# Kernel optimization log

Measured on AMD Instinct MI355X. Metric: run time of the kernel, lower is better.

The kernel has to match this reference:

```python
import jax, jax.numpy as jnp
import numpy as np

UNITS = 1024
NUM_HEADS = 8


def setup_inputs() -> dict:
    key = jax.random.key(0)
    k1, k2, k3 = jax.random.split(key, 3)
    B, S = 8, 1024
    memory = jax.random.normal(k1, (B, S, 2 * UNITS), dtype=jnp.float32)
    query = jax.random.normal(k2, (B, S, UNITS), dtype=jnp.float32)
    seq_mask = jax.random.randint(k3, (B, S), 0, 2, dtype=jnp.int32)
    b = jnp.zeros((1,), dtype=jnp.float32)  # learned scalar bias added to logits
    return {"memory": memory, "query": query, "seq_mask": seq_mask, "b": b}


def _split_heads(x, n):
    # [B, S, D] -> [B, n, S, D//n]
    B, S, D = x.shape
    return x.reshape(B, S, n, D // n).transpose(0, 2, 1, 3)


def reference(memory, query, seq_mask, b):
    H = NUM_HEADS
    depth = UNITS // H
    Q = _split_heads(query, H) * (depth ** -0.5)          # [B,H,S,d]
    k_mem, v_mem = jnp.split(memory, 2, axis=2)
    K = _split_heads(k_mem, H)                            # [B,H,S,d]
    V = _split_heads(v_mem, H)                            # [B,H,S,d]
    logits = jnp.einsum('bhqd,bhkd->bhqk', Q, K) + b[0]   # [B,H,S,S]
    mask = seq_mask.astype(jnp.float32)[:, None, None, :]  # [B,1,1,S]
    logits = logits + (-1e30) * (1.0 - mask)
    weights = jax.nn.softmax(logits, axis=-1)
    out = jnp.einsum('bhqk,bhkd->bhqd', weights, V)       # [B,H,S,d]
    B, _, S, _ = out.shape
    return out.transpose(0, 2, 1, 3).reshape(B, S, UNITS)
```

## Files before the change

### kernel.cpp

```cpp
#include <hip/hip_runtime.h>
#include <stdint.h>


typedef __attribute__((ext_vector_type(8))) short bf16x8;
typedef __attribute__((ext_vector_type(4))) float f32x4;
typedef __attribute__((ext_vector_type(16))) float f32x16;
typedef __attribute__((ext_vector_type(4))) unsigned int u32x4;

#define NB 8
#define SS 1024
#define NH 8
#define DH 128
#define BM 128
#define BN 64
#define KPAD 136
#define VPAD 72
#define NT (SS / BN)

__device__ __forceinline__ unsigned short f2bf(float f) {
    unsigned int u = __builtin_bit_cast(unsigned int, f);
    u += 0x7fffu + ((u >> 16) & 1u);
    return (unsigned short)(u >> 16);
}

__device__ __forceinline__ unsigned int cvt_pk_bf16(float lo, float hi) {
#if __has_builtin(__builtin_amdgcn_cvt_pk_bf16_f32)
    typedef __attribute__((ext_vector_type(2))) __bf16 bf16x2_t;
    bf16x2_t r = __builtin_amdgcn_cvt_pk_bf16_f32(lo, hi);
    return __builtin_bit_cast(unsigned int, r);
#else
    return (unsigned int)f2bf(lo) | ((unsigned int)f2bf(hi) << 16);
#endif
}

__device__ __forceinline__ void bar_lgkm() {
    asm volatile("s_waitcnt lgkmcnt(0)" ::: "memory");
    __builtin_amdgcn_s_barrier();
    asm volatile("" ::: "memory");
}

__device__ __forceinline__ void pswap(unsigned int &a, unsigned int &b) {
#if __has_builtin(__builtin_amdgcn_permlane32_swap)
    auto r = __builtin_amdgcn_permlane32_swap(a, b, false, false);
    a = (unsigned int)r[0];
    b = (unsigned int)r[1];
#else
    unsigned int sa = (unsigned int)__shfl_xor((int)a, 32, 64);
    unsigned int sb = (unsigned int)__shfl_xor((int)b, 32, 64);
    const bool hh = (threadIdx.x & 32) != 0;
    unsigned int na = hh ? sb : a;
    unsigned int nb = hh ? b : sa;
    a = na; b = nb;
#endif
}

__global__ __launch_bounds__(256, 2)
void attn_flash(const float* __restrict__ mem,
                const float* __restrict__ query,
                const int* __restrict__ seq_mask,
                float* __restrict__ out)
{
    __shared__ unsigned short K_lds[2][BN * KPAD];
    __shared__ unsigned short Vt_lds[2][DH * VPAD];

    const int tid  = threadIdx.x;
    const int wave = tid >> 6;
    const int lane = tid & 63;
    const int hi   = lane >> 5;
    const int l31  = lane & 31;

    const int bh = blockIdx.x;
    const int b  = bh >> 3;
    const int h  = bh & 7;
    const int q0w = blockIdx.y * BM + wave * 32;

    bf16x8 qf[8];
    {
        const float* qb = query + ((size_t)(b * SS + q0w + l31) << 10) + h * DH + hi * 8;
        #pragma unroll
        for (int dep = 0; dep < 8; ++dep) {
            f32x4 lo = *(const f32x4*)(qb + dep * 16);
            f32x4 ho = *(const f32x4*)(qb + dep * 16 + 4);
            u32x4 q;
            q[0] = cvt_pk_bf16(lo[0], lo[1]);
            q[1] = cvt_pk_bf16(lo[2], lo[3]);
            q[2] = cvt_pk_bf16(ho[0], ho[1]);
            q[3] = cvt_pk_bf16(ho[2], ho[3]);
            qf[dep] = __builtin_bit_cast(bf16x8, q);
        }
    }

    f32x16 acc[4];
    #pragma unroll
    for (int dt = 0; dt < 4; ++dt)
        #pragma unroll
        for (int i = 0; i < 16; ++i) acc[dt][i] = 0.f;
    float l_i = 0.f;

    const float cs = 0.12752789747141537f;

    const int krow = tid >> 4;
    const int kcc  = (tid & 15) * 8;
    const int vq   = tid & 31;
    const int vg8  = tid >> 5;

    const float* kbase = mem + ((size_t)(b * SS) << 11) + h * DH;
    const float* vbase = kbase + 1024;
    const int* mbase = seq_mask + b * SS;

    f32x4 pka[4], pkb[4];
    f32x4 pva0[2], pva1[2], pvb0[2], pvb1[2];
    int pmv, pmv_next;

    #pragma unroll
    for (int it = 0; it < 4; ++it) {
        const float* src = kbase + ((size_t)(it * 16 + krow) << 11) + kcc;
        pka[it] = *(const f32x4*)src;
        pkb[it] = *(const f32x4*)(src + 4);
    }
    #pragma unroll
    for (int task = 0; task < 2; ++task) {
        int d0 = vg8 * 8 + task * 64;
        const float* pa = vbase + ((size_t)(2 * vq) << 11) + d0;
        pva0[task] = *(const f32x4*)pa;
        pva1[task] = *(const f32x4*)(pa + 4);
        pvb0[task] = *(const f32x4*)(pa + 2048);
        pvb1[task] = *(const f32x4*)(pa + 2048 + 4);
    }
    pmv = mbase[lane];

    #pragma unroll
    for (int it = 0; it < 4; ++it) {
        u32x4 t;
        t[0] = cvt_pk_bf16(pka[it][0], pka[it][1]);
        t[1] = cvt_pk_bf16(pka[it][2], pka[it][3]);
        t[2] = cvt_pk_bf16(pkb[it][0], pkb[it][1]);
        t[3] = cvt_pk_bf16(pkb[it][2], pkb[it][3]);
        *(u32x4*)&K_lds[0][(it * 16 + krow) * KPAD + kcc] = t;
    }
    #pragma unroll
    for (int task = 0; task < 2; ++task) {
        int d0 = vg8 * 8 + task * 64;
        #pragma unroll
        for (int j = 0; j < 8; ++j) {
            float av = (j < 4) ? pva0[task][j] : pva1[task][j - 4];
            float bv = (j < 4) ? pvb0[task][j] : pvb1[task][j - 4];
            *(unsigned int*)&Vt_lds[0][(d0 + j) * VPAD + 2 * vq] =
                cvt_pk_bf16(av, bv);
        }
    }

    #pragma unroll
    for (int it = 0; it < 4; ++it) {
        const float* src = kbase + ((size_t)(BN + it * 16 + krow) << 11) + kcc;
        pka[it] = *(const f32x4*)src;
        pkb[it] = *(const f32x4*)(src + 4);
    }
    #pragma unroll
    for (int task = 0; task < 2; ++task) {
        int d0 = vg8 * 8 + task * 64;
        const float* pa = vbase + ((size_t)(BN + 2 * vq) << 11) + d0;
        pva0[task] = *(const f32x4*)pa;
        pva1[task] = *(const f32x4*)(pa + 4);
        pvb0[task] = *(const f32x4*)(pa + 2048);
        pvb1[task] = *(const f32x4*)(pa + 2048 + 4);
    }
    pmv_next = mbase[BN + lane];

    bar_lgkm();

    for (int kt = 0; kt < NT; ++kt) {
        const int cur = kt & 1;
        const unsigned short* Kc = &K_lds[cur][0];
        const unsigned short* Vc = &Vt_lds[cur][0];

        const unsigned long long bmask = __ballot(pmv != 0);
        const unsigned int wsh0 = (unsigned int)(bmask >> (4 * hi));
        const unsigned int wsh1 = (unsigned int)(bmask >> (32 + 4 * hi));

        #pragma unroll
        for (int jt = 0; jt < 2; ++jt) {
            const unsigned int mword = jt ? wsh1 : wsh0;

            f32x16 s;
            #pragma unroll
            for (int i = 0; i < 16; ++i) s[i] = 0.f;
            __builtin_amdgcn_s_setprio(1);
            #pragma unroll
            for (int dep = 0; dep < 8; ++dep) {
                bf16x8 kf = *(const bf16x8*)&Kc[(jt * 32 + l31) * KPAD + dep * 16 + hi * 8];
                s = __builtin_amdgcn_mfma_f32_32x32x16_bf16(kf, qf[dep], s, 0, 0, 0);
            }
            __builtin_amdgcn_s_setprio(0);

            float p[16];
            #pragma unroll
            for (int r = 0; r < 16; ++r) {
                const int sr = (r & 3) + 8 * (r >> 2);
                float e = __builtin_amdgcn_exp2f(s[r] * cs);
                float m = (float)((mword >> sr) & 1u);
                p[r] = e * m;
            }
            {
                float t0 = (p[0] + p[1]) + (p[2] + p[3]);
                float t1 = (p[4] + p[5]) + (p[6] + p[7]);
                float t2 = (p[8] + p[9]) + (p[10] + p[11]);
                float t3 = (p[12] + p[13]) + (p[14] + p[15]);
                l_i += (t0 + t1) + (t2 + t3);
            }

            unsigned int w[8];
            #pragma unroll
            for (int i = 0; i < 8; ++i) w[i] = cvt_pk_bf16(p[2 * i], p[2 * i + 1]);
            pswap(w[0], w[2]); pswap(w[1], w[3]);
            pswap(w[4], w[6]); pswap(w[5], w[7]);
            bf16x8 af0 = __builtin_bit_cast(bf16x8, (u32x4){w[0], w[1], w[2], w[3]});
            bf16x8 af1 = __builtin_bit_cast(bf16x8, (u32x4){w[4], w[5], w[6], w[7]});

            __builtin_amdgcn_s_setprio(1);
            #pragma unroll
            for (int ksl = 0; ksl < 2; ++ksl) {
                bf16x8 ap = ksl ? af1 : af0;
                #pragma unroll
                for (int dt = 0; dt < 4; ++dt) {
                    bf16x8 bv = *(const bf16x8*)&Vc[(dt * 32 + l31) * VPAD +
                                                    jt * 32 + ksl * 16 + hi * 8];
                    acc[dt] = __builtin_amdgcn_mfma_f32_32x32x16_bf16(ap, bv, acc[dt], 0, 0, 0);
                }
            }
            __builtin_amdgcn_s_setprio(0);
        }

        if (kt < NT - 1) {
            unsigned short* Kn = &K_lds[cur ^ 1][0];
            unsigned short* Vn = &Vt_lds[cur ^ 1][0];
            #pragma unroll
            for (int it = 0; it < 4; ++it) {
                u32x4 t;
                t[0] = cvt_pk_bf16(pka[it][0], pka[it][1]);
                t[1] = cvt_pk_bf16(pka[it][2], pka[it][3]);
                t[2] = cvt_pk_bf16(pkb[it][0], pkb[it][1]);
                t[3] = cvt_pk_bf16(pkb[it][2], pkb[it][3]);
                *(u32x4*)&Kn[(it * 16 + krow) * KPAD + kcc] = t;
            }
            #pragma unroll
            for (int task = 0; task < 2; ++task) {
                int d0 = vg8 * 8 + task * 64;
                #pragma unroll
                for (int j = 0; j < 8; ++j) {
                    float av = (j < 4) ? pva0[task][j] : pva1[task][j - 4];
                    float bv = (j < 4) ? pvb0[task][j] : pvb1[task][j - 4];
                    *(unsigned int*)&Vn[(d0 + j) * VPAD + 2 * vq] =
                        cvt_pk_bf16(av, bv);
                }
            }

            const int kk2 = (kt < NT - 2) ? (kt + 2) * BN : (kt + 1) * BN;
            #pragma unroll
            for (int it = 0; it < 4; ++it) {
                const float* src = kbase + ((size_t)(kk2 + it * 16 + krow) << 11) + kcc;
                pka[it] = *(const f32x4*)src;
                pkb[it] = *(const f32x4*)(src + 4);
            }
            #pragma unroll
            for (int task = 0; task < 2; ++task) {
                int d0 = vg8 * 8 + task * 64;
                const float* pa = vbase + ((size_t)(kk2 + 2 * vq) << 11) + d0;
                pva0[task] = *(const f32x4*)pa;
                pva1[task] = *(const f32x4*)(pa + 4);
                pvb0[task] = *(const f32x4*)(pa + 2048);
                pvb1[task] = *(const f32x4*)(pa + 2048 + 4);
            }
            pmv = pmv_next;
            pmv_next = mbase[kk2 + lane];

            bar_lgkm();
        }
    }

    float lt = l_i + __shfl_xor(l_i, 32, 64);
    float invl = 1.f / lt;
    #pragma unroll
    for (int r = 0; r < 16; ++r) {
        const int qrow = (r & 3) + 8 * (r >> 2) + 4 * hi;
        float iv = __shfl(invl, qrow, 64);
        float* ob = out + ((size_t)(b * SS + q0w + qrow) << 10) + h * DH + l31;
        #pragma unroll
        for (int dt = 0; dt < 4; ++dt)
            ob[dt * 32] = acc[dt][r] * iv;
    }
}

extern "C" void kernel_launch(void* const* d_in, const int* in_sizes, int n_in,
                              void* d_out, int out_size, void* d_ws, size_t ws_size,
                              hipStream_t stream)
{
    (void)in_sizes; (void)n_in; (void)d_ws; (void)ws_size; (void)out_size;
    const float* mem    = (const float*)d_in[0];
    const float* query  = (const float*)d_in[1];
    const int* seq_mask = (const int*)d_in[2];
    dim3 grid(NB * NH, SS / BM);
    attn_flash<<<grid, 256, 0, stream>>>(mem, query, seq_mask, (float*)d_out);
}
```

Baseline: 176.2 us.

## Move key masking into V tiles and compute softmax denominator via MFMA

Masked keys are now handled by zeroing their V rows in LDS and storing a bf16 0/1 mask vector in LDS. The per-element mask multiply and scalar row-sum reduction are replaced by an extra MFMA of P against the mask vector, which yields the denominator directly in the output layout. The two QK^T MFMA chains are also interleaved for more ILP. The cost is one extra MFMA per slice and extra registers for the second score tile and the denominator accumulator. The denominator now sums bf16-rounded probabilities, which changes numerics slightly.

```diff
diff --git a/kernel.cpp b/kernel.cpp
--- a/kernel.cpp
+++ b/kernel.cpp
@@ -62,6 +62,7 @@
 {
     __shared__ unsigned short K_lds[2][BN * KPAD];
     __shared__ unsigned short Vt_lds[2][DH * VPAD];
+    __shared__ __align__(16) unsigned short m_lds[2][64];
 
     const int tid  = threadIdx.x;
     const int wave = tid >> 6;
@@ -95,7 +96,9 @@
     for (int dt = 0; dt < 4; ++dt)
         #pragma unroll
         for (int i = 0; i < 16; ++i) acc[dt][i] = 0.f;
-    float l_i = 0.f;
+    f32x16 acc_l;
+    #pragma unroll
+    for (int i = 0; i < 16; ++i) acc_l[i] = 0.f;
 
     const float cs = 0.12752789747141537f;
 
@@ -110,7 +113,7 @@
 
     f32x4 pka[4], pkb[4];
     f32x4 pva0[2], pva1[2], pvb0[2], pvb1[2];
-    int pmv, pmv_next;
+    int pm;
 
     #pragma unroll
     for (int it = 0; it < 4; ++it) {
@@ -127,7 +130,7 @@
         pvb0[task] = *(const f32x4*)(pa + 2048);
         pvb1[task] = *(const f32x4*)(pa + 2048 + 4);
     }
-    pmv = mbase[lane];
+    pm = mbase[lane];
 
     #pragma unroll
     for (int it = 0; it < 4; ++it) {
@@ -138,16 +141,23 @@
         t[3] = cvt_pk_bf16(pkb[it][2], pkb[it][3]);
         *(u32x4*)&K_lds[0][(it * 16 + krow) * KPAD + kcc] = t;
     }
-    #pragma unroll
-    for (int task = 0; task < 2; ++task) {
-        int d0 = vg8 * 8 + task * 64;
-        #pragma unroll
-        for (int j = 0; j < 8; ++j) {
-            float av = (j < 4) ? pva0[task][j] : pva1[task][j - 4];
-            float bv = (j < 4) ? pvb0[task][j] : pvb1[task][j - 4];
-            *(unsigned int*)&Vt_lds[0][(d0 + j) * VPAD + 2 * vq] =
-                cvt_pk_bf16(av, bv);
-        }
+    {
+        unsigned long long bmn = __ballot(pm != 0);
+        unsigned int mm = (unsigned int)(bmn >> (2 * vq));
+        unsigned int vmask = ((mm & 1u) ? 0xffffu : 0u) | ((mm & 2u) ? 0xffff0000u : 0u);
+        #pragma unroll
+        for (int task = 0; task < 2; ++task) {
+            int d0 = vg8 * 8 + task * 64;
+            #pragma unroll
+            for (int j = 0; j < 8; ++j) {
+                float av = (j < 4) ? pva0[task][j] : pva1[task][j - 4];
+                float bv = (j < 4) ? pvb0[task][j] : pvb1[task][j - 4];
+                *(unsigned int*)&Vt_lds[0][(d0 + j) * VPAD + 2 * vq] =
+                    cvt_pk_bf16(av, bv) & vmask;
+            }
+        }
+        if (wave == 0)
+            m_lds[0][lane] = pm ? (unsigned short)0x3F80 : (unsigned short)0;
     }
 
     #pragma unroll
@@ -165,7 +175,7 @@
         pvb0[task] = *(const f32x4*)(pa + 2048);
         pvb1[task] = *(const f32x4*)(pa + 2048 + 4);
     }
-    pmv_next = mbase[BN + lane];
+    pm = mbase[BN + lane];
 
     bar_lgkm();
 
@@ -173,54 +183,58 @@
         const int cur = kt & 1;
         const unsigned short* Kc = &K_lds[cur][0];
         const unsigned short* Vc = &Vt_lds[cur][0];
-
-        const unsigned long long bmask = __ballot(pmv != 0);
-        const unsigned int wsh0 = (unsigned int)(bmask >> (4 * hi));
-        const unsigned int wsh1 = (unsigned int)(bmask >> (32 + 4 * hi));
-
+        const unsigned short* Mc = &m_lds[cur][0];
+
+        f32x16 s0, s1;
+        #pragma unroll
+        for (int i = 0; i < 16; ++i) { s0[i] = 0.f; s1[i] = 0.f; }
+        __builtin_amdgcn_s_setprio(1);
+        #pragma unroll
+        for (int dep = 0; dep < 8; ++dep) {
+            bf16x8 k0 = *(const bf16x8*)&Kc[(l31)      * KPAD + dep * 16 + hi * 8];
+            bf16x8 k1 = *(const bf16x8*)&Kc[(32 + l31) * KPAD + dep * 16 + hi * 8];
+            s0 = __builtin_amdgcn_mfma_f32_32x32x16_bf16(k0, qf[dep], s0, 0, 0, 0);
+            s1 = __builtin_amdgcn_mfma_f32_32x32x16_bf16(k1, qf[dep], s1, 0, 0, 0);
+        }
+        __builtin_amdgcn_s_setprio(0);
+
+        bf16x8 mf[2][2];
+        #pragma unroll
+        for (int jt = 0; jt < 2; ++jt)
+            #pragma unroll
+            for (int ksl = 0; ksl < 2; ++ksl)
+                mf[jt][ksl] = *(const bf16x8*)&Mc[jt * 32 + ksl * 16 + hi * 8];
+
+        float p0[16], p1[16];
+        #pragma unroll
+        for (int r = 0; r < 16; ++r) {
+            p0[r] = __builtin_amdgcn_exp2f(s0[r] * cs);
+            p1[r] = __builtin_amdgcn_exp2f(s1[r] * cs);
+        }
+
+        unsigned int w0[8], w1[8];
+        #pragma unroll
+        for (int i = 0; i < 8; ++i) {
+            w0[i] = cvt_pk_bf16(p0[2 * i], p0[2 * i + 1]);
+            w1[i] = cvt_pk_bf16(p1[2 * i], p1[2 * i + 1]);
+        }
+        pswap(w0[0], w0[2]); pswap(w0[1], w0[3]);
+        pswap(w0[4], w0[6]); pswap(w0[5], w0[7]);
+        pswap(w1[0], w1[2]); pswap(w1[1], w1[3]);
+        pswap(w1[4], w1[6]); pswap(w1[5], w1[7]);
+        bf16x8 af[2][2];
+        af[0][0] = __builtin_bit_cast(bf16x8, (u32x4){w0[0], w0[1], w0[2], w0[3]});
+        af[0][1] = __builtin_bit_cast(bf16x8, (u32x4){w0[4], w0[5], w0[6], w0[7]});
+        af[1][0] = __builtin_bit_cast(bf16x8, (u32x4){w1[0], w1[1], w1[2], w1[3]});
+        af[1][1] = __builtin_bit_cast(bf16x8, (u32x4){w1[4], w1[5], w1[6], w1[7]});
+
+        __builtin_amdgcn_s_setprio(1);
         #pragma unroll
         for (int jt = 0; jt < 2; ++jt) {
-            const unsigned int mword = jt ? wsh1 : wsh0;
-
-            f32x16 s;
-            #pragma unroll
-            for (int i = 0; i < 16; ++i) s[i] = 0.f;
-            __builtin_amdgcn_s_setprio(1);
-            #pragma unroll
-            for (int dep = 0; dep < 8; ++dep) {
-                bf16x8 kf = *(const bf16x8*)&Kc[(jt * 32 + l31) * KPAD + dep * 16 + hi * 8];
-                s = __builtin_amdgcn_mfma_f32_32x32x16_bf16(kf, qf[dep], s, 0, 0, 0);
-            }
-            __builtin_amdgcn_s_setprio(0);
-
-            float p[16];
-            #pragma unroll
-            for (int r = 0; r < 16; ++r) {
-                const int sr = (r & 3) + 8 * (r >> 2);
-                float e = __builtin_amdgcn_exp2f(s[r] * cs);
-                float m = (float)((mword >> sr) & 1u);
-                p[r] = e * m;
-            }
-            {
-                float t0 = (p[0] + p[1]) + (p[2] + p[3]);
-                float t1 = (p[4] + p[5]) + (p[6] + p[7]);
-                float t2 = (p[8] + p[9]) + (p[10] + p[11]);
-                float t3 = (p[12] + p[13]) + (p[14] + p[15]);
-                l_i += (t0 + t1) + (t2 + t3);
-            }
-
-            unsigned int w[8];
-            #pragma unroll
-            for (int i = 0; i < 8; ++i) w[i] = cvt_pk_bf16(p[2 * i], p[2 * i + 1]);
-            pswap(w[0], w[2]); pswap(w[1], w[3]);
-            pswap(w[4], w[6]); pswap(w[5], w[7]);
-            bf16x8 af0 = __builtin_bit_cast(bf16x8, (u32x4){w[0], w[1], w[2], w[3]});
-            bf16x8 af1 = __builtin_bit_cast(bf16x8, (u32x4){w[4], w[5], w[6], w[7]});
-
-            __builtin_amdgcn_s_setprio(1);
             #pragma unroll
             for (int ksl = 0; ksl < 2; ++ksl) {
-                bf16x8 ap = ksl ? af1 : af0;
+                bf16x8 ap = af[jt][ksl];
+                acc_l = __builtin_amdgcn_mfma_f32_32x32x16_bf16(ap, mf[jt][ksl], acc_l, 0, 0, 0);
                 #pragma unroll
                 for (int dt = 0; dt < 4; ++dt) {
                     bf16x8 bv = *(const bf16x8*)&Vc[(dt * 32 + l31) * VPAD +
@@ -228,8 +242,8 @@
                     acc[dt] = __builtin_amdgcn_mfma_f32_32x32x16_bf16(ap, bv, acc[dt], 0, 0, 0);
                 }
             }
-            __builtin_amdgcn_s_setprio(0);
-        }
+        }
+        __builtin_amdgcn_s_setprio(0);
 
         if (kt < NT - 1) {
             unsigned short* Kn = &K_lds[cur ^ 1][0];
@@ -243,16 +257,23 @@
                 t[3] = cvt_pk_bf16(pkb[it][2], pkb[it][3]);
                 *(u32x4*)&Kn[(it * 16 + krow) * KPAD + kcc] = t;
             }
-            #pragma unroll
-            for (int task = 0; task < 2; ++task) {
-                int d0 = vg8 * 8 + task * 64;
+            {
+                unsigned long long bmn = __ballot(pm != 0);
+                unsigned int mm = (unsigned int)(bmn >> (2 * vq));
+                unsigned int vmask = ((mm & 1u) ? 0xffffu : 0u) | ((mm & 2u) ? 0xffff0000u : 0u);
                 #pragma unroll
-                for (int j = 0; j < 8; ++j) {
-                    float av = (j < 4) ? pva0[task][j] : pva1[task][j - 4];
-                    float bv = (j < 4) ? pvb0[task][j] : pvb1[task][j - 4];
-                    *(unsigned int*)&Vn[(d0 + j) * VPAD + 2 * vq] =
-                        cvt_pk_bf16(av, bv);
+                for (int task = 0; task < 2; ++task) {
+                    int d0 = vg8 * 8 + task * 64;
+                    #pragma unroll
+                    for (int j = 0; j < 8; ++j) {
+                        float av = (j < 4) ? pva0[task][j] : pva1[task][j - 4];
+                        float bv = (j < 4) ? pvb0[task][j] : pvb1[task][j - 4];
+                        *(unsigned int*)&Vn[(d0 + j) * VPAD + 2 * vq] =
+                            cvt_pk_bf16(av, bv) & vmask;
+                    }
                 }
+                if (wave == 0)
+                    m_lds[cur ^ 1][lane] = pm ? (unsigned short)0x3F80 : (unsigned short)0;
             }
 
             const int kk2 = (kt < NT - 2) ? (kt + 2) * BN : (kt + 1) * BN;
@@ -271,19 +292,16 @@
                 pvb0[task] = *(const f32x4*)(pa + 2048);
                 pvb1[task] = *(const f32x4*)(pa + 2048 + 4);
             }
-            pmv = pmv_next;
-            pmv_next = mbase[kk2 + lane];
+            pm = mbase[kk2 + lane];
 
             bar_lgkm();
         }
     }
 
-    float lt = l_i + __shfl_xor(l_i, 32, 64);
-    float invl = 1.f / lt;
     #pragma unroll
     for (int r = 0; r < 16; ++r) {
         const int qrow = (r & 3) + 8 * (r >> 2) + 4 * hi;
-        float iv = __shfl(invl, qrow, 64);
+        float iv = 1.f / acc_l[r];
         float* ob = out + ((size_t)(b * SS + q0w + qrow) << 10) + h * DH + l31;
         #pragma unroll
         for (int dt = 0; dt < 4; ++dt)
```

Measured after the change: 197.0 us. 11.9% more time.
